# Optimization experiments

Measured on AMD Instinct MI355X. Metric: run time of the kernel, lower is better.

The kernel has to match this reference:

```python
import jax, jax.numpy as jnp
import numpy as np

D_EDGE = 64


def segment_mean(feats, idx, num_segments):
    # feats: [E, d], idx: [E] int -> [num_segments, d] mean-aggregated
    s = jax.ops.segment_sum(feats, idx, num_segments=num_segments)
    cnt = jax.ops.segment_sum(jnp.ones((feats.shape[0],), feats.dtype), idx,
                              num_segments=num_segments)
    return s / jnp.maximum(cnt, 1.0)[:, None]


def setup_inputs() -> dict:
    key = jax.random.key(0)
    k1, k2, k3, k4, k5, k6 = jax.random.split(key, 6)
    N = 50000
    E = 800000
    Es = 400000
    edge_index = jax.random.randint(k1, (2, E), 0, N, dtype=jnp.int64 if jax.config.read('jax_enable_x64') else jnp.int32)
    same_frame_edge_index = jax.random.randint(k2, (2, Es), 0, N, dtype=edge_index.dtype)
    edge_attr = jax.random.normal(k3, (E, D_EDGE), dtype=jnp.float32)
    same_frame_edge_attr = jax.random.normal(k4, (Es, D_EDGE), dtype=jnp.float32)
    W1 = jax.random.normal(k5, (3 * D_EDGE, 128), dtype=jnp.float32) * (1.0 / np.sqrt(3 * D_EDGE))
    b1 = jnp.zeros((128,), jnp.float32)
    W2 = jax.random.normal(k6, (128, 64), dtype=jnp.float32) * (1.0 / np.sqrt(128))
    b2 = jnp.zeros((64,), jnp.float32)
    return {"edge_index": edge_index, "edge_attr": edge_attr, "num_nodes": N,
            "same_frame_edge_index": same_frame_edge_index,
            "same_frame_edge_attr": same_frame_edge_attr,
            "W1": W1, "b1": b1, "W2": W2, "b2": b2}


def reference(edge_index, edge_attr, num_nodes, same_frame_edge_index,
              same_frame_edge_attr, W1, b1, W2, b2):
    past_nodes, future_nodes = edge_index[0], edge_index[1]
    early, later = same_frame_edge_index[0], same_frame_edge_index[1]
    fwd_agg = segment_mean(edge_attr, future_nodes, num_nodes)   # [N, d]
    bwd_agg = segment_mean(edge_attr, past_nodes, num_nodes)     # [N, d]
    # vstack duplicates same-frame attrs; indices concat both directions
    sf_attr = jnp.concatenate([same_frame_edge_attr, same_frame_edge_attr], axis=0)
    sf_idx = jnp.concatenate([early, later], axis=0)
    frame_agg = segment_mean(sf_attr, sf_idx, num_nodes)         # [N, d]
    flow_total = jnp.concatenate([fwd_agg, frame_agg, bwd_agg], axis=1)  # [N, 3d]
    h = jax.nn.relu(flow_total @ W1 + b1)
    return h @ W2 + b2
```

## Files before the change

kernel.cpp:

```cpp
#include <hip/hip_runtime.h>
#include <hip/hip_bf16.h>
#include <cstdint>


#define D 64
#define R_BITS 6
#define R 64
#define CAP 2048
#define NB_MAX 4096
#define TILE_SRC 2048

__global__ __launch_bounds__(256) void bin_kernel(
    const int* __restrict__ ei, const int* __restrict__ sfi,
    int* __restrict__ bucket_cur, unsigned int* __restrict__ binned,
    int E, int Es, int N, int NB)
{
    __shared__ int hist[NB_MAX];
    __shared__ int base_sh[NB_MAX];

    int t = threadIdx.x;
    int tile0 = blockIdx.x * TILE_SRC;

    for (int b = t; b < NB; b += 256) hist[b] = 0;
    __syncthreads();

#pragma unroll
    for (int u = 0; u < 8; ++u) {
        int src = tile0 + u * 256 + t;
        if (src < E) {
            atomicAdd(&hist[((unsigned)ei[E + src]) >> R_BITS], 1);
            atomicAdd(&hist[((unsigned)(2 * N + ei[src])) >> R_BITS], 1);
        } else if (src < E + Es) {
            int e = src - E;
            atomicAdd(&hist[((unsigned)(N + sfi[e])) >> R_BITS], 1);
            atomicAdd(&hist[((unsigned)(N + sfi[Es + e])) >> R_BITS], 1);
        }
    }
    __syncthreads();

    for (int b = t; b < NB; b += 256) {
        int c = hist[b];
        base_sh[b] = (c > 0) ? atomicAdd(&bucket_cur[b], c) : 0;
        hist[b] = 0;
    }
    __syncthreads();

#pragma unroll
    for (int u = 0; u < 8; ++u) {
        int src = tile0 + u * 256 + t;
        if (src >= E + Es) continue;
        unsigned int g0, g1, e;
        if (src < E) {
            e = (unsigned)src;
            g0 = (unsigned)ei[E + src];
            g1 = (unsigned)(2 * N + ei[src]);
        } else {
            e = (unsigned)(src - E);
            g0 = (unsigned)(N + sfi[e]);
            g1 = (unsigned)(N + sfi[Es + e]);
        }
        int b0 = g0 >> R_BITS, b1 = g1 >> R_BITS;
        int r0 = base_sh[b0] + atomicAdd(&hist[b0], 1);
        if (r0 < CAP) binned[(size_t)b0 * CAP + r0] = ((g0 & (R - 1)) << 20) | e;
        int r1 = base_sh[b1] + atomicAdd(&hist[b1], 1);
        if (r1 < CAP) binned[(size_t)b1 * CAP + r1] = ((g1 & (R - 1)) << 20) | e;
    }
}

__global__ __launch_bounds__(256) void gather_sort_kernel(
    const float* __restrict__ edge_attr, const float* __restrict__ sf_attr,
    const unsigned int* __restrict__ binned, const int* __restrict__ bucket_cur,
    float* __restrict__ flow, int N, int T)
{
    __shared__ unsigned int stage[CAP];
    __shared__ unsigned int slist[CAP];
    __shared__ int kcnt[R];
    __shared__ int kstart[R];
    __shared__ int kcur[R];

    int b = blockIdx.x;
    int t = threadIdx.x;
    int w = t >> 6;
    int lane = t & 63;
    int slot = lane >> 4;
    int quad = lane & 15;

    if (t < R) kcnt[t] = 0;
    __syncthreads();

    int cb = bucket_cur[b];
    if (cb > CAP) cb = CAP;

    for (int i = t; i < cb; i += 256) {
        unsigned int p = binned[(size_t)b * CAP + i];
        stage[i] = p;
        atomicAdd(&kcnt[p >> 20], 1);
    }
    __syncthreads();

    if (t < R) {
        int c = kcnt[t];
        int v = c;
#pragma unroll
        for (int d = 1; d < 64; d <<= 1) {
            int x = __shfl_up(v, d);
            if (t >= d) v += x;
        }
        kstart[t] = v - c;
        kcur[t]   = v - c;
    }
    __syncthreads();

    for (int i = t; i < cb; i += 256) {
        unsigned int p = stage[i];
        int r = atomicAdd(&kcur[p >> 20], 1);
        slist[r] = p & 0xFFFFFu;
    }
    __syncthreads();

    for (int kk = w * 16; kk < w * 16 + 16; ++kk) {
        int g = (b << R_BITS) + kk;
        if (g >= T) break;
        int s = (g >= 2 * N) ? 2 : ((g >= N) ? 1 : 0);
        int node = g - s * N;
        const float4* attr4 =
            reinterpret_cast<const float4*>((s == 1) ? sf_attr : edge_attr);

        int start = kstart[kk];
        int deg   = kcnt[kk];
        int end   = start + deg;

        float ax = 0.f, ay = 0.f, az = 0.f, aw = 0.f;
        int k = start;
        for (; k + 16 <= end; k += 16) {
            unsigned int e0 = slist[k + slot];
            unsigned int e1 = slist[k + 4 + slot];
            unsigned int e2 = slist[k + 8 + slot];
            unsigned int e3 = slist[k + 12 + slot];
            float4 v0 = attr4[(size_t)e0 * 16 + quad];
            float4 v1 = attr4[(size_t)e1 * 16 + quad];
            float4 v2 = attr4[(size_t)e2 * 16 + quad];
            float4 v3 = attr4[(size_t)e3 * 16 + quad];
            ax += v0.x + v1.x + v2.x + v3.x;
            ay += v0.y + v1.y + v2.y + v3.y;
            az += v0.z + v1.z + v2.z + v3.z;
            aw += v0.w + v1.w + v2.w + v3.w;
        }
        for (; k + 8 <= end; k += 8) {
            unsigned int e0 = slist[k + slot];
            unsigned int e1 = slist[k + 4 + slot];
            float4 v0 = attr4[(size_t)e0 * 16 + quad];
            float4 v1 = attr4[(size_t)e1 * 16 + quad];
            ax += v0.x + v1.x; ay += v0.y + v1.y;
            az += v0.z + v1.z; aw += v0.w + v1.w;
        }
        if (k + 4 <= end) {
            unsigned int e0 = slist[k + slot];
            float4 v0 = attr4[(size_t)e0 * 16 + quad];
            ax += v0.x; ay += v0.y; az += v0.z; aw += v0.w;
            k += 4;
        }
        if (k + slot < end) {
            unsigned int e0 = slist[k + slot];
            float4 v0 = attr4[(size_t)e0 * 16 + quad];
            ax += v0.x; ay += v0.y; az += v0.z; aw += v0.w;
        }

        ax += __shfl_xor(ax, 16); ay += __shfl_xor(ay, 16);
        az += __shfl_xor(az, 16); aw += __shfl_xor(aw, 16);
        ax += __shfl_xor(ax, 32); ay += __shfl_xor(ay, 32);
        az += __shfl_xor(az, 32); aw += __shfl_xor(aw, 32);

        if (slot == 0) {
            float inv = 1.0f / fmaxf((float)deg, 1.0f);
            float4 o = make_float4(ax * inv, ay * inv, az * inv, aw * inv);
            reinterpret_cast<float4*>(flow)[(size_t)node * 48 + s * 16 + quad] = o;
        }
    }
}

#define MLP_NODES 64
#define LDS_PITCH 65

__global__ __launch_bounds__(256) void mlp_kernel(
    const float* __restrict__ flow,
    const float* __restrict__ W1, const float* __restrict__ b1,
    const float* __restrict__ W2, const float* __restrict__ b2,
    float* __restrict__ out, int N)
{
    __shared__ float lds[192 * LDS_PITCH];

    int t = threadIdx.x;
    int nbase = blockIdx.x * MLP_NODES;

    const float4* flow4 = reinterpret_cast<const float4*>(flow);
    for (int idx = t; idx < MLP_NODES * 48; idx += 256) {
        int ln = idx / 48;
        int q  = idx - ln * 48;
        int node = nbase + ln;
        float4 v = make_float4(0.f, 0.f, 0.f, 0.f);
        if (node < N) v = flow4[(size_t)node * 48 + q];
        int i = q * 4;
        lds[(i + 0) * LDS_PITCH + ln] = v.x;
        lds[(i + 1) * LDS_PITCH + ln] = v.y;
        lds[(i + 2) * LDS_PITCH + ln] = v.z;
        lds[(i + 3) * LDS_PITCH + ln] = v.w;
    }
    __syncthreads();

    int tn = t & 15;
    int tc = t >> 4;
    int n0 = tn * 4;
    int c0 = tc * 8;

    float acc[4][8];
#pragma unroll
    for (int a = 0; a < 4; ++a)
#pragma unroll
        for (int b = 0; b < 8; ++b) acc[a][b] = 0.0f;

    for (int i = 0; i < 192; ++i) {
        float4 fv = *reinterpret_cast<const float4*>(&lds[i * LDS_PITCH + n0]);
        float4 wa = *reinterpret_cast<const float4*>(&W1[i * 128 + c0]);
        float4 wb = *reinterpret_cast<const float4*>(&W1[i * 128 + c0 + 4]);
        float f[4] = {fv.x, fv.y, fv.z, fv.w};
        float w[8] = {wa.x, wa.y, wa.z, wa.w, wb.x, wb.y, wb.z, wb.w};
#pragma unroll
        for (int a = 0; a < 4; ++a)
#pragma unroll
            for (int b = 0; b < 8; ++b)
                acc[a][b] += f[a] * w[b];
    }
    __syncthreads();

#pragma unroll
    for (int b = 0; b < 8; ++b) {
        int col = c0 + b;
        float bias = b1[col];
        float4 hv;
        hv.x = fmaxf(acc[0][b] + bias, 0.0f);
        hv.y = fmaxf(acc[1][b] + bias, 0.0f);
        hv.z = fmaxf(acc[2][b] + bias, 0.0f);
        hv.w = fmaxf(acc[3][b] + bias, 0.0f);
        *reinterpret_cast<float4*>(&lds[col * LDS_PITCH + n0]) = hv;
    }
    __syncthreads();

    int c20 = tc * 4;
    float acc2[4][4];
#pragma unroll
    for (int a = 0; a < 4; ++a)
#pragma unroll
        for (int b = 0; b < 4; ++b) acc2[a][b] = 0.0f;

    for (int i = 0; i < 128; ++i) {
        float4 hv = *reinterpret_cast<const float4*>(&lds[i * LDS_PITCH + n0]);
        float4 wv = *reinterpret_cast<const float4*>(&W2[i * 64 + c20]);
        float h[4] = {hv.x, hv.y, hv.z, hv.w};
        float w[4] = {wv.x, wv.y, wv.z, wv.w};
#pragma unroll
        for (int a = 0; a < 4; ++a)
#pragma unroll
            for (int b = 0; b < 4; ++b)
                acc2[a][b] += h[a] * w[b];
    }

    float4 bb = *reinterpret_cast<const float4*>(&b2[c20]);
#pragma unroll
    for (int a = 0; a < 4; ++a) {
        int node = nbase + n0 + a;
        if (node < N) {
            float4 o;
            o.x = acc2[a][0] + bb.x;
            o.y = acc2[a][1] + bb.y;
            o.z = acc2[a][2] + bb.z;
            o.w = acc2[a][3] + bb.w;
            *reinterpret_cast<float4*>(&out[(size_t)node * D + c20]) = o;
        }
    }
}

extern "C" void kernel_launch(void* const* d_in, const int* in_sizes, int n_in,
                              void* d_out, int out_size, void* d_ws, size_t ws_size,
                              hipStream_t stream)
{
    const int*   edge_index = (const int*)d_in[0];
    const float* edge_attr  = (const float*)d_in[1];
    const int*   sf_index   = (const int*)d_in[3];
    const float* sf_attr    = (const float*)d_in[4];
    const float* W1         = (const float*)d_in[5];
    const float* b1         = (const float*)d_in[6];
    const float* W2         = (const float*)d_in[7];
    const float* b2         = (const float*)d_in[8];
    float* out = (float*)d_out;

    int E  = in_sizes[0] / 2;
    int Es = in_sizes[3] / 2;
    int N  = out_size / D;
    int T  = 3 * N;
    int NB = (T + R - 1) / R;

    float* flow = (float*)d_ws;
    size_t flow_elems = (size_t)N * 192;

    unsigned int* binned = (unsigned int*)(flow + flow_elems);
    int* bucket_cur = (int*)(binned + (size_t)NB * CAP);

    hipMemsetAsync(bucket_cur, 0, (size_t)NB * sizeof(int), stream);

    int nsrc = E + Es;
    int bin_blocks = (nsrc + TILE_SRC - 1) / TILE_SRC;

    bin_kernel<<<bin_blocks, 256, 0, stream>>>(
        edge_index, sf_index, bucket_cur, binned, E, Es, N, NB);

    gather_sort_kernel<<<NB, 256, 0, stream>>>(
        edge_attr, sf_attr, binned, bucket_cur, flow, N, T);

    {
        int blocks = (N + MLP_NODES - 1) / MLP_NODES;
        mlp_kernel<<<blocks, 256, 0, stream>>>(flow, W1, b1, W2, b2, out, N);
    }
}
```

Baseline: 241.7 us.

## Use bf16 MFMA for MLP with bf16 flow buffer and larger bin tiles

Replaces the scalar fp32 two-layer MLP with bf16 MFMA 16x16x32 instructions. Weights are converted and transposed to bf16 by a small new kernel, and the aggregated flow features are written as bf16, which halves their storage and traffic. It also doubles the source tile size in the binning kernel. Precision drops to bf16 inputs with fp32 accumulation, and one extra kernel launch is added.

```diff
diff --git a/kernel.cpp b/kernel.cpp
--- a/kernel.cpp
+++ b/kernel.cpp
@@ -8,7 +8,32 @@
 #define R 64
 #define CAP 2048
 #define NB_MAX 4096
-#define TILE_SRC 2048
+#define TILE_SRC 4096
+
+typedef __attribute__((ext_vector_type(8))) short bf16x8;
+typedef __attribute__((ext_vector_type(4))) float f32x4;
+
+__device__ inline unsigned short f2bf(float x) {
+    unsigned int u = __float_as_uint(x);
+    unsigned int r = u + 0x7FFFu + ((u >> 16) & 1u);
+    return (unsigned short)(r >> 16);
+}
+
+__global__ __launch_bounds__(256) void wconv_kernel(
+    const float* __restrict__ W1, const float* __restrict__ W2,
+    unsigned short* __restrict__ W1T, unsigned short* __restrict__ W2T)
+{
+    int i = blockIdx.x * 256 + threadIdx.x;
+    if (i < 192 * 128) {
+        int k = i >> 7, n = i & 127;
+        W1T[n * 192 + k] = f2bf(W1[i]);
+    }
+    int j = i - 192 * 128;
+    if (j >= 0 && j < 128 * 64) {
+        int k = j >> 6, n = j & 63;
+        W2T[n * 128 + k] = f2bf(W2[j]);
+    }
+}
 
 __global__ __launch_bounds__(256) void bin_kernel(
     const int* __restrict__ ei, const int* __restrict__ sfi,
@@ -25,7 +50,7 @@
     __syncthreads();
 
 #pragma unroll
-    for (int u = 0; u < 8; ++u) {
+    for (int u = 0; u < 16; ++u) {
         int src = tile0 + u * 256 + t;
         if (src < E) {
             atomicAdd(&hist[((unsigned)ei[E + src]) >> R_BITS], 1);
@@ -46,7 +71,7 @@
     __syncthreads();
 
 #pragma unroll
-    for (int u = 0; u < 8; ++u) {
+    for (int u = 0; u < 16; ++u) {
         int src = tile0 + u * 256 + t;
         if (src >= E + Es) continue;
         unsigned int g0, g1, e;
@@ -70,7 +95,7 @@
 __global__ __launch_bounds__(256) void gather_sort_kernel(
     const float* __restrict__ edge_attr, const float* __restrict__ sf_attr,
     const unsigned int* __restrict__ binned, const int* __restrict__ bucket_cur,
-    float* __restrict__ flow, int N, int T)
+    unsigned short* __restrict__ flow, int N, int T)
 {
     __shared__ unsigned int stage[CAP];
     __shared__ unsigned int slist[CAP];
@@ -173,109 +198,103 @@
 
         if (slot == 0) {
             float inv = 1.0f / fmaxf((float)deg, 1.0f);
-            float4 o = make_float4(ax * inv, ay * inv, az * inv, aw * inv);
-            reinterpret_cast<float4*>(flow)[(size_t)node * 48 + s * 16 + quad] = o;
+            ushort4 o;
+            o.x = f2bf(ax * inv);
+            o.y = f2bf(ay * inv);
+            o.z = f2bf(az * inv);
+            o.w = f2bf(aw * inv);
+            *reinterpret_cast<ushort4*>(
+                &flow[(size_t)node * 192 + s * D + quad * 4]) = o;
         }
     }
 }
 
 #define MLP_NODES 64
-#define LDS_PITCH 65
+#define FP 200
+#define HP 136
 
 __global__ __launch_bounds__(256) void mlp_kernel(
-    const float* __restrict__ flow,
-    const float* __restrict__ W1, const float* __restrict__ b1,
-    const float* __restrict__ W2, const float* __restrict__ b2,
+    const unsigned short* __restrict__ flow,
+    const unsigned short* __restrict__ W1T,
+    const float* __restrict__ b1,
+    const unsigned short* __restrict__ W2T,
+    const float* __restrict__ b2,
     float* __restrict__ out, int N)
 {
-    __shared__ float lds[192 * LDS_PITCH];
+    __shared__ unsigned short ldsf[MLP_NODES * FP];
+    __shared__ unsigned short ldsh[MLP_NODES * HP];
 
     int t = threadIdx.x;
     int nbase = blockIdx.x * MLP_NODES;
 
-    const float4* flow4 = reinterpret_cast<const float4*>(flow);
-    for (int idx = t; idx < MLP_NODES * 48; idx += 256) {
-        int ln = idx / 48;
-        int q  = idx - ln * 48;
-        int node = nbase + ln;
-        float4 v = make_float4(0.f, 0.f, 0.f, 0.f);
-        if (node < N) v = flow4[(size_t)node * 48 + q];
-        int i = q * 4;
-        lds[(i + 0) * LDS_PITCH + ln] = v.x;
-        lds[(i + 1) * LDS_PITCH + ln] = v.y;
-        lds[(i + 2) * LDS_PITCH + ln] = v.z;
-        lds[(i + 3) * LDS_PITCH + ln] = v.w;
-    }
-    __syncthreads();
-
-    int tn = t & 15;
-    int tc = t >> 4;
-    int n0 = tn * 4;
-    int c0 = tc * 8;
-
-    float acc[4][8];
-#pragma unroll
-    for (int a = 0; a < 4; ++a)
-#pragma unroll
-        for (int b = 0; b < 8; ++b) acc[a][b] = 0.0f;
-
-    for (int i = 0; i < 192; ++i) {
-        float4 fv = *reinterpret_cast<const float4*>(&lds[i * LDS_PITCH + n0]);
-        float4 wa = *reinterpret_cast<const float4*>(&W1[i * 128 + c0]);
-        float4 wb = *reinterpret_cast<const float4*>(&W1[i * 128 + c0 + 4]);
-        float f[4] = {fv.x, fv.y, fv.z, fv.w};
-        float w[8] = {wa.x, wa.y, wa.z, wa.w, wb.x, wb.y, wb.z, wb.w};
-#pragma unroll
-        for (int a = 0; a < 4; ++a)
-#pragma unroll
-            for (int b = 0; b < 8; ++b)
-                acc[a][b] += f[a] * w[b];
-    }
-    __syncthreads();
-
-#pragma unroll
-    for (int b = 0; b < 8; ++b) {
-        int col = c0 + b;
+    for (int i = t; i < 1536; i += 256) {
+        int node = i / 24;
+        int q    = i - node * 24;
+        uint4 v = make_uint4(0u, 0u, 0u, 0u);
+        if (nbase + node < N)
+            v = *reinterpret_cast<const uint4*>(&flow[(size_t)(nbase + node) * 192 + q * 8]);
+        *reinterpret_cast<uint4*>(&ldsf[node * FP + q * 8]) = v;
+    }
+    __syncthreads();
+
+    int w   = t >> 6;
+    int l   = t & 63;
+    int m16 = l & 15;
+    int kg  = l >> 4;
+
+    f32x4 acc[8];
+#pragma unroll
+    for (int i = 0; i < 8; ++i) acc[i] = (f32x4){0.f, 0.f, 0.f, 0.f};
+
+#pragma unroll
+    for (int kt = 0; kt < 6; ++kt) {
+        bf16x8 a = *reinterpret_cast<const bf16x8*>(
+            &ldsf[(w * 16 + m16) * FP + kt * 32 + kg * 8]);
+#pragma unroll
+        for (int nt = 0; nt < 8; ++nt) {
+            bf16x8 bfr = *reinterpret_cast<const bf16x8*>(
+                &W1T[(size_t)(nt * 16 + m16) * 192 + kt * 32 + kg * 8]);
+            acc[nt] = __builtin_amdgcn_mfma_f32_16x16x32_bf16(a, bfr, acc[nt], 0, 0, 0);
+        }
+    }
+
+#pragma unroll
+    for (int nt = 0; nt < 8; ++nt) {
+        int col = nt * 16 + m16;
         float bias = b1[col];
-        float4 hv;
-        hv.x = fmaxf(acc[0][b] + bias, 0.0f);
-        hv.y = fmaxf(acc[1][b] + bias, 0.0f);
-        hv.z = fmaxf(acc[2][b] + bias, 0.0f);
-        hv.w = fmaxf(acc[3][b] + bias, 0.0f);
-        *reinterpret_cast<float4*>(&lds[col * LDS_PITCH + n0]) = hv;
-    }
-    __syncthreads();
-
-    int c20 = tc * 4;
-    float acc2[4][4];
-#pragma unroll
-    for (int a = 0; a < 4; ++a)
-#pragma unroll
-        for (int b = 0; b < 4; ++b) acc2[a][b] = 0.0f;
-
-    for (int i = 0; i < 128; ++i) {
-        float4 hv = *reinterpret_cast<const float4*>(&lds[i * LDS_PITCH + n0]);
-        float4 wv = *reinterpret_cast<const float4*>(&W2[i * 64 + c20]);
-        float h[4] = {hv.x, hv.y, hv.z, hv.w};
-        float w[4] = {wv.x, wv.y, wv.z, wv.w};
-#pragma unroll
-        for (int a = 0; a < 4; ++a)
-#pragma unroll
-            for (int b = 0; b < 4; ++b)
-                acc2[a][b] += h[a] * w[b];
-    }
-
-    float4 bb = *reinterpret_cast<const float4*>(&b2[c20]);
-#pragma unroll
-    for (int a = 0; a < 4; ++a) {
-        int node = nbase + n0 + a;
-        if (node < N) {
-            float4 o;
-            o.x = acc2[a][0] + bb.x;
-            o.y = acc2[a][1] + bb.y;
-            o.z = acc2[a][2] + bb.z;
-            o.w = acc2[a][3] + bb.w;
-            *reinterpret_cast<float4*>(&out[(size_t)node * D + c20]) = o;
+#pragma unroll
+        for (int r = 0; r < 4; ++r) {
+            int node = w * 16 + kg * 4 + r;
+            ldsh[node * HP + col] = f2bf(fmaxf(acc[nt][r] + bias, 0.f));
+        }
+    }
+    __syncthreads();
+
+    f32x4 acc2[4];
+#pragma unroll
+    for (int i = 0; i < 4; ++i) acc2[i] = (f32x4){0.f, 0.f, 0.f, 0.f};
+
+#pragma unroll
+    for (int kt = 0; kt < 4; ++kt) {
+        bf16x8 a = *reinterpret_cast<const bf16x8*>(
+            &ldsh[(w * 16 + m16) * HP + kt * 32 + kg * 8]);
+#pragma unroll
+        for (int nt = 0; nt < 4; ++nt) {
+            bf16x8 bfr = *reinterpret_cast<const bf16x8*>(
+                &W2T[(size_t)(nt * 16 + m16) * 128 + kt * 32 + kg * 8]);
+            acc2[nt] = __builtin_amdgcn_mfma_f32_16x16x32_bf16(a, bfr, acc2[nt], 0, 0, 0);
+        }
+    }
+
+#pragma unroll
+    for (int nt = 0; nt < 4; ++nt) {
+        int col = nt * 16 + m16;
+        float bias = b2[col];
+#pragma unroll
+        for (int r = 0; r < 4; ++r) {
+            int node = nbase + w * 16 + kg * 4 + r;
+            if (node < N)
+                out[(size_t)node * D + col] = acc2[nt][r] + bias;
         }
     }
 }
@@ -300,13 +319,18 @@
     int T  = 3 * N;
     int NB = (T + R - 1) / R;
 
-    float* flow = (float*)d_ws;
+    unsigned short* flow = (unsigned short*)d_ws;
     size_t flow_elems = (size_t)N * 192;
 
     unsigned int* binned = (unsigned int*)(flow + flow_elems);
     int* bucket_cur = (int*)(binned + (size_t)NB * CAP);
+    unsigned short* W1T = (unsigned short*)(bucket_cur + NB_MAX);
+    unsigned short* W2T = W1T + 128 * 192;
 
     hipMemsetAsync(bucket_cur, 0, (size_t)NB * sizeof(int), stream);
+
+    wconv_kernel<<<(192 * 128 + 128 * 64 + 255) / 256, 256, 0, stream>>>(
+        W1, W2, W1T, W2T);
 
     int nsrc = E + Es;
     int bin_blocks = (nsrc + TILE_SRC - 1) / TILE_SRC;
@@ -319,6 +343,6 @@
 
     {
         int blocks = (N + MLP_NODES - 1) / MLP_NODES;
-        mlp_kernel<<<blocks, 256, 0, stream>>>(flow, W1, b1, W2, b2, out, N);
-    }
-}
+        mlp_kernel<<<blocks, 256, 0, stream>>>(flow, W1T, b1, W2T, b2, out, N);
+    }
+}
```

After: 202.0 us. 16.4% less time.
